# Kernel tuning notes

Hardware: AMD Instinct MI355X
Metric: run time of the kernel (lower is better)

Reference implementation:

```python
import jax, jax.numpy as jnp
import numpy as np

B, IN, H, NOPT = 16384, 4096, 128, 64
GAIN = 0.5  # default control_gains value in the module


def gru_cell(x, h, Wih, Whh, bih, bhh):
    # torch GRU single step; gate order r, z, n
    gi = x @ Wih + bih          # [B, 3H]
    gh = h @ Whh + bhh          # [B, 3H]
    ir, iz, inn = jnp.split(gi, 3, axis=-1)
    hr, hz, hn = jnp.split(gh, 3, axis=-1)
    r = jax.nn.sigmoid(ir + hr)
    z = jax.nn.sigmoid(iz + hz)
    n = jnp.tanh(inn + r * hn)
    return (1.0 - z) * n + z * h


def setup_inputs() -> dict:
    key = jax.random.key(0)
    ks = jax.random.split(key, 12)
    s = lambda k, shape: (jax.random.normal(k, shape, jnp.float32) * 0.05)
    return {
        "obs": jax.random.normal(ks[0], (B, IN), jnp.float32),
        "chosen_option": jax.random.randint(ks[1], (B,), 0, NOPT),
        "h0": jnp.zeros((B, H), jnp.float32),
        "h1": jnp.zeros((B, H), jnp.float32),
        "Wa": s(ks[2], (IN, H)), "ba": jnp.zeros((H,), jnp.float32),
        "Wih0": s(ks[3], (H, 3 * H)), "Whh0": s(ks[4], (H, 3 * H)),
        "bih0": jnp.zeros((3 * H,), jnp.float32), "bhh0": jnp.zeros((3 * H,), jnp.float32),
        "Wih1": s(ks[5], (2 * H, 3 * H)), "Whh1": s(ks[6], (H, 3 * H)),
        "bih1": jnp.zeros((3 * H,), jnp.float32), "bhh1": jnp.zeros((3 * H,), jnp.float32),
        "Wv0": s(ks[7], (H, NOPT)), "bv0": jnp.zeros((NOPT,), jnp.float32),
        "Wv1": s(ks[8], (H, NOPT)), "bv1": jnp.zeros((NOPT,), jnp.float32),
        "Wt0": s(ks[9], (H, NOPT)), "bt0": jnp.zeros((NOPT,), jnp.float32),
    }


def reference(obs, chosen_option, h0, h1, Wa, ba, Wih0, Whh0, bih0, bhh0,
              Wih1, Whh1, bih1, bhh1, Wv0, bv0, Wv1, bv1, Wt0, bt0):
    # attention: tanh(Linear(obs))
    attn = jnp.tanh(obs @ Wa + ba)                       # [B, H]
    # layer 0: GRU on attn
    h0n = gru_cell(attn, h0, Wih0, Whh0, bih0, bhh0)     # [B, H]
    hc0 = (h0n - 0.5) * GAIN + 0.5                       # gain contrast
    v0 = hc0 @ Wv0 + bv0                                 # [B, NOPT]
    term = jax.nn.sigmoid(hc0 @ Wt0 + bt0)               # [B, NOPT]
    term_p = jnp.take_along_axis(term, chosen_option[:, None], axis=1)  # [B, 1]
    # layer 1: GRU on cat(attn, own hidden)
    x1 = jnp.concatenate([attn, h1], axis=-1)            # [B, 2H]
    h1n = gru_cell(x1, h1, Wih1, Whh1, bih1, bhh1)       # [B, H]
    hc1 = (h1n - 0.5) * GAIN + 0.5
    v1 = hc1 @ Wv1 + bv1                                 # [B, NOPT]
    return v0, term_p, v1, h0n, h1n
```

## Files before the change

kernel.cpp:

```cpp
#include <hip/hip_runtime.h>
#include <stdint.h>


typedef __attribute__((ext_vector_type(8))) short bf16x8;
typedef __attribute__((ext_vector_type(4))) float f32x4;
typedef __attribute__((ext_vector_type(4))) float f4;
typedef __attribute__((ext_vector_type(4))) unsigned short u16x4;

#define INDIM 4096
#define H 128
#define NOPT 64

#define WS_WAT    0u
#define WS_WIH0T  524288u
#define WS_WHH0T  573440u
#define WS_WIH1T  622592u
#define WS_WHH1T  720896u
#define WS_WV0T   770048u
#define WS_WV1T   778240u
#define WS_WT0T   786432u
#define WS_ATTN   794624u

#define OUT_V0    0u
#define OUT_TERMP 1048576u
#define OUT_V1    1064960u
#define OUT_H0N   2113536u
#define OUT_H1N   4210688u

static __device__ __forceinline__ float bf2f(uint16_t u) {
  union { uint32_t i; float f; } x; x.i = ((uint32_t)u) << 16; return x.f;
}
static __device__ __forceinline__ uint16_t f2bf(float f) {
  union { float f; uint32_t i; } x; x.f = f;
  uint32_t r = x.i + 0x7fffu + ((x.i >> 16) & 1u);
  return (uint16_t)(r >> 16);
}
static __device__ __forceinline__ float sigm(float x) { return 1.0f / (1.0f + __expf(-x)); }
static __device__ __forceinline__ float fast_tanh(float x) {
  float e = __expf(2.0f * x);
  return 1.0f - 2.0f / (e + 1.0f);
}
static __device__ __forceinline__ f32x4 mfma16(bf16x8 a, bf16x8 b, f32x4 c) {
  return __builtin_amdgcn_mfma_f32_16x16x32_bf16(a, b, c, 0, 0, 0);
}
static __device__ __forceinline__ u16x4 pack4(f4 v) {
  u16x4 p;
  p[0] = f2bf(v[0]); p[1] = f2bf(v[1]); p[2] = f2bf(v[2]); p[3] = f2bf(v[3]);
  return p;
}

__global__ void k_transpose(const float* __restrict__ Wa,
                            const float* __restrict__ Wih0,
                            const float* __restrict__ Whh0,
                            const float* __restrict__ Wih1,
                            const float* __restrict__ Whh1,
                            const float* __restrict__ Wv0,
                            const float* __restrict__ Wv1,
                            const float* __restrict__ Wt0,
                            uint16_t* __restrict__ ws) {
  int blk = blockIdx.x;
  const float* in; uint16_t* out; int ksh; int N; int base;
  if (blk < 2048)      { in = Wa;   out = ws + WS_WAT;   ksh = 12; N = 128; base = 0; }
  else if (blk < 2240) { in = Wih0; out = ws + WS_WIH0T; ksh = 7;  N = 384; base = 2048; }
  else if (blk < 2432) { in = Whh0; out = ws + WS_WHH0T; ksh = 7;  N = 384; base = 2240; }
  else if (blk < 2816) { in = Wih1; out = ws + WS_WIH1T; ksh = 8;  N = 384; base = 2432; }
  else if (blk < 3008) { in = Whh1; out = ws + WS_WHH1T; ksh = 7;  N = 384; base = 2816; }
  else if (blk < 3040) { in = Wv0;  out = ws + WS_WV0T;  ksh = 7;  N = 64;  base = 3008; }
  else if (blk < 3072) { in = Wv1;  out = ws + WS_WV1T;  ksh = 7;  N = 64;  base = 3040; }
  else                 { in = Wt0;  out = ws + WS_WT0T;  ksh = 7;  N = 64;  base = 3072; }
  int e = (blk - base) * 256 + (int)threadIdx.x;
  int n = e >> ksh;
  int k = e & ((1 << ksh) - 1);
  out[e] = f2bf(in[(size_t)k * N + n]);
}

__launch_bounds__(128)
__global__ void k_attn(const float* __restrict__ obs,
                       uint16_t* __restrict__ ws,
                       const float* __restrict__ ba) {
  __shared__ uint16_t sA[32 * 64];
  __shared__ uint16_t sB[128 * 64];
  const uint16_t* WaT = ws + WS_WAT;
  uint16_t* attn = ws + WS_ATTN;
  const int t = threadIdx.x, w = t >> 6, lane = t & 63;
  const int l15 = lane & 15, quad = lane >> 4;
  const int row0 = blockIdx.x * 32;
  f32x4 acc[8] = {};
  const int rA = 16 * w + l15;
  for (int kt = 0; kt < 64; ++kt) {
    const int k0 = kt * 64;
    f4 va[4]; bf16x8 vb[8];
#pragma unroll
    for (int i = 0; i < 4; ++i) {
      int p = i * 128 + t, r = p >> 4, kb4 = p & 15;
      va[i] = *(const f4*)(obs + (size_t)(row0 + r) * INDIM + k0 + kb4 * 4);
    }
#pragma unroll
    for (int i = 0; i < 8; ++i) {
      int p = i * 128 + t, n = p >> 3, kb = p & 7;
      vb[i] = *(const bf16x8*)(WaT + (size_t)n * INDIM + k0 + kb * 8);
    }
    __syncthreads();
#pragma unroll
    for (int i = 0; i < 4; ++i) {
      int p = i * 128 + t, r = p >> 4, kb4 = p & 15;
      int c8 = (kb4 >> 1) ^ (r & 7);
      *(u16x4*)&sA[(r * 8 + c8) * 8 + (kb4 & 1) * 4] = pack4(va[i]);
    }
#pragma unroll
    for (int i = 0; i < 8; ++i) {
      int p = i * 128 + t, n = p >> 3, kb = p & 7;
      *(bf16x8*)&sB[(n * 8 + (kb ^ (n & 7))) * 8] = vb[i];
    }
    __syncthreads();
#pragma unroll
    for (int ks = 0; ks < 2; ++ks) {
      const int kb = ks * 4 + quad;
      bf16x8 a = *(const bf16x8*)&sA[(rA * 8 + (kb ^ (rA & 7))) * 8];
#pragma unroll
      for (int nb = 0; nb < 8; ++nb) {
        int nB = nb * 16 + l15;
        bf16x8 b = *(const bf16x8*)&sB[(nB * 8 + (kb ^ (nB & 7))) * 8];
        acc[nb] = mfma16(a, b, acc[nb]);
      }
    }
  }
#pragma unroll
  for (int nb = 0; nb < 8; ++nb) {
    int col = nb * 16 + l15;
    float bav = ba[col];
#pragma unroll
    for (int i = 0; i < 4; ++i) {
      int grow = row0 + 16 * w + quad * 4 + i;
      attn[(size_t)grow * H + col] = f2bf(fast_tanh(acc[nb][i] + bav));
    }
  }
}

__launch_bounds__(128)
__global__ void k_gru0(const uint16_t* __restrict__ ws,
                       const float* __restrict__ h0,
                       const float* __restrict__ bih0,
                       const float* __restrict__ bhh0,
                       const float* __restrict__ bv0,
                       const float* __restrict__ bt0,
                       const int* __restrict__ chosen,
                       float* __restrict__ out) {
  __shared__ uint16_t sX[32 * 128];
  __shared__ uint16_t sH[32 * 128];
  __shared__ uint16_t sC[32 * 128];
  const uint16_t* attn = ws + WS_ATTN;
  const uint16_t* WihT = ws + WS_WIH0T;
  const uint16_t* WhhT = ws + WS_WHH0T;
  const uint16_t* WvT  = ws + WS_WV0T;
  const uint16_t* WtT  = ws + WS_WT0T;
  const int t = threadIdx.x, w = t >> 6, lane = t & 63;
  const int l15 = lane & 15, quad = lane >> 4;
  const int row0 = blockIdx.x * 32;
  {
    bf16x8 vx[4]; f4 vh[8];
#pragma unroll
    for (int i = 0; i < 4; ++i) {
      int p = i * 128 + t, r = p >> 4, kb = p & 15;
      vx[i] = *(const bf16x8*)(attn + (size_t)(row0 + r) * H + kb * 8);
    }
#pragma unroll
    for (int i = 0; i < 8; ++i) {
      int p = i * 128 + t, r = p >> 5, kb4 = p & 31;
      vh[i] = *(const f4*)(h0 + (size_t)(row0 + r) * H + kb4 * 4);
    }
#pragma unroll
    for (int i = 0; i < 4; ++i) {
      int p = i * 128 + t, r = p >> 4, kb = p & 15;
      *(bf16x8*)&sX[(r * 16 + (kb ^ (r & 15))) * 8] = vx[i];
    }
#pragma unroll
    for (int i = 0; i < 8; ++i) {
      int p = i * 128 + t, r = p >> 5, kb4 = p & 31;
      int c8 = (kb4 >> 1) ^ (r & 15);
      *(u16x4*)&sH[(r * 16 + c8) * 8 + (kb4 & 1) * 4] = pack4(vh[i]);
    }
  }
  __syncthreads();
  const int rA = 16 * w + l15;
  bf16x8 ax[4], ah[4];
#pragma unroll
  for (int ks = 0; ks < 4; ++ks) {
    int kb = ks * 4 + quad;
    int sl = rA * 16 + (kb ^ (rA & 15));
    ax[ks] = *(const bf16x8*)&sX[sl * 8];
    ah[ks] = *(const bf16x8*)&sH[sl * 8];
  }
#pragma unroll
  for (int nb = 0; nb < 8; ++nb) {
    f32x4 air = {}, ahr = {}, aiz = {}, ahz = {}, ain = {}, ahn = {};
    int nrow = nb * 16 + l15;
#pragma unroll
    for (int ks = 0; ks < 4; ++ks) {
      int k = ks * 32 + quad * 8;
      bf16x8 b;
      b = *(const bf16x8*)(WihT + (size_t)(nrow      ) * H + k); air = mfma16(ax[ks], b, air);
      b = *(const bf16x8*)(WihT + (size_t)(nrow + 128) * H + k); aiz = mfma16(ax[ks], b, aiz);
      b = *(const bf16x8*)(WihT + (size_t)(nrow + 256) * H + k); ain = mfma16(ax[ks], b, ain);
      b = *(const bf16x8*)(WhhT + (size_t)(nrow      ) * H + k); ahr = mfma16(ah[ks], b, ahr);
      b = *(const bf16x8*)(WhhT + (size_t)(nrow + 128) * H + k); ahz = mfma16(ah[ks], b, ahz);
      b = *(const bf16x8*)(WhhT + (size_t)(nrow + 256) * H + k); ahn = mfma16(ah[ks], b, ahn);
    }
    int col = nb * 16 + l15;
    float b_ir = bih0[col],       b_hr = bhh0[col];
    float b_iz = bih0[col + 128], b_hz = bhh0[col + 128];
    float b_in = bih0[col + 256], b_hn = bhh0[col + 256];
    int slc = col >> 3;
#pragma unroll
    for (int i = 0; i < 4; ++i) {
      int r = 16 * w + quad * 4 + i;
      int grow = row0 + r;
      float rr = sigm(air[i] + ahr[i] + b_ir + b_hr);
      float zz = sigm(aiz[i] + ahz[i] + b_iz + b_hz);
      float nn = fast_tanh(ain[i] + b_in + rr * (ahn[i] + b_hn));
      float hv = bf2f(sH[(r * 16 + (slc ^ (r & 15))) * 8 + (col & 7)]);
      float hnew = (1.0f - zz) * nn + zz * hv;
      out[OUT_H0N + (size_t)grow * H + col] = hnew;
      sC[(r * 16 + (slc ^ (r & 15))) * 8 + (col & 7)] = f2bf(0.5f * hnew + 0.25f);
    }
  }
  __syncthreads();
  bf16x8 ac[4];
#pragma unroll
  for (int ks = 0; ks < 4; ++ks) {
    int kb = ks * 4 + quad;
    ac[ks] = *(const bf16x8*)&sC[(rA * 16 + (kb ^ (rA & 15))) * 8];
  }
#pragma unroll
  for (int vb = 0; vb < 4; ++vb) {
    f32x4 av = {}, at = {};
    int nrow = vb * 16 + l15;
#pragma unroll
    for (int ks = 0; ks < 4; ++ks) {
      int k = ks * 32 + quad * 8;
      bf16x8 b;
      b = *(const bf16x8*)(WvT + (size_t)nrow * H + k); av = mfma16(ac[ks], b, av);
      b = *(const bf16x8*)(WtT + (size_t)nrow * H + k); at = mfma16(ac[ks], b, at);
    }
    int col = vb * 16 + l15;
    float bvv = bv0[col], btv = bt0[col];
#pragma unroll
    for (int i = 0; i < 4; ++i) {
      int grow = row0 + 16 * w + quad * 4 + i;
      out[OUT_V0 + (size_t)grow * NOPT + col] = av[i] + bvv;
      if (chosen[grow] == col)
        out[OUT_TERMP + grow] = sigm(at[i] + btv);
    }
  }
}

__launch_bounds__(128)
__global__ void k_gru1(const uint16_t* __restrict__ ws,
                       const float* __restrict__ h1,
                       const float* __restrict__ bih1,
                       const float* __restrict__ bhh1,
                       const float* __restrict__ bv1,
                       float* __restrict__ out) {
  __shared__ uint16_t sX[32 * 128];
  __shared__ uint16_t sH[32 * 128];
  __shared__ uint16_t sC[32 * 128];
  const uint16_t* attn  = ws + WS_ATTN;
  const uint16_t* WihT  = ws + WS_WIH1T;
  const uint16_t* WhhT  = ws + WS_WHH1T;
  const uint16_t* WvT   = ws + WS_WV1T;
  const int t = threadIdx.x, w = t >> 6, lane = t & 63;
  const int l15 = lane & 15, quad = lane >> 4;
  const int row0 = blockIdx.x * 32;
  {
    bf16x8 vx[4]; f4 vh[8];
#pragma unroll
    for (int i = 0; i < 4; ++i) {
      int p = i * 128 + t, r = p >> 4, kb = p & 15;
      vx[i] = *(const bf16x8*)(attn + (size_t)(row0 + r) * H + kb * 8);
    }
#pragma unroll
    for (int i = 0; i < 8; ++i) {
      int p = i * 128 + t, r = p >> 5, kb4 = p & 31;
      vh[i] = *(const f4*)(h1 + (size_t)(row0 + r) * H + kb4 * 4);
    }
#pragma unroll
    for (int i = 0; i < 4; ++i) {
      int p = i * 128 + t, r = p >> 4, kb = p & 15;
      *(bf16x8*)&sX[(r * 16 + (kb ^ (r & 15))) * 8] = vx[i];
    }
#pragma unroll
    for (int i = 0; i < 8; ++i) {
      int p = i * 128 + t, r = p >> 5, kb4 = p & 31;
      int c8 = (kb4 >> 1) ^ (r & 15);
      *(u16x4*)&sH[(r * 16 + c8) * 8 + (kb4 & 1) * 4] = pack4(vh[i]);
    }
  }
  __syncthreads();
  const int rA = 16 * w + l15;
  bf16x8 ax[4], ah[4];
#pragma unroll
  for (int ks = 0; ks < 4; ++ks) {
    int kb = ks * 4 + quad;
    int sl = rA * 16 + (kb ^ (rA & 15));
    ax[ks] = *(const bf16x8*)&sX[sl * 8];
    ah[ks] = *(const bf16x8*)&sH[sl * 8];
  }
#pragma unroll
  for (int nb = 0; nb < 8; ++nb) {
    f32x4 air = {}, ahr = {}, aiz = {}, ahz = {}, ain = {}, ahn = {};
    int nrow = nb * 16 + l15;
#pragma unroll
    for (int ks = 0; ks < 8; ++ks) {
      int k = ks * 32 + quad * 8;
      bf16x8 a = (ks < 4) ? ax[ks] : ah[ks - 4];
      bf16x8 b;
      b = *(const bf16x8*)(WihT + (size_t)(nrow      ) * 256 + k); air = mfma16(a, b, air);
      b = *(const bf16x8*)(WihT + (size_t)(nrow + 128) * 256 + k); aiz = mfma16(a, b, aiz);
      b = *(const bf16x8*)(WihT + (size_t)(nrow + 256) * 256 + k); ain = mfma16(a, b, ain);
    }
#pragma unroll
    for (int ks = 0; ks < 4; ++ks) {
      int k = ks * 32 + quad * 8;
      bf16x8 b;
      b = *(const bf16x8*)(WhhT + (size_t)(nrow      ) * H + k); ahr = mfma16(ah[ks], b, ahr);
      b = *(const bf16x8*)(WhhT + (size_t)(nrow + 128) * H + k); ahz = mfma16(ah[ks], b, ahz);
      b = *(const bf16x8*)(WhhT + (size_t)(nrow + 256) * H + k); ahn = mfma16(ah[ks], b, ahn);
    }
    int col = nb * 16 + l15;
    float b_ir = bih1[col],       b_hr = bhh1[col];
    float b_iz = bih1[col + 128], b_hz = bhh1[col + 128];
    float b_in = bih1[col + 256], b_hn = bhh1[col + 256];
    int slc = col >> 3;
#pragma unroll
    for (int i = 0; i < 4; ++i) {
      int r = 16 * w + quad * 4 + i;
      int grow = row0 + r;
      float rr = sigm(air[i] + ahr[i] + b_ir + b_hr);
      float zz = sigm(aiz[i] + ahz[i] + b_iz + b_hz);
      float nn = fast_tanh(ain[i] + b_in + rr * (ahn[i] + b_hn));
      float hv = bf2f(sH[(r * 16 + (slc ^ (r & 15))) * 8 + (col & 7)]);
      float hnew = (1.0f - zz) * nn + zz * hv;
      out[OUT_H1N + (size_t)grow * H + col] = hnew;
      sC[(r * 16 + (slc ^ (r & 15))) * 8 + (col & 7)] = f2bf(0.5f * hnew + 0.25f);
    }
  }
  __syncthreads();
  bf16x8 ac[4];
#pragma unroll
  for (int ks = 0; ks < 4; ++ks) {
    int kb = ks * 4 + quad;
    ac[ks] = *(const bf16x8*)&sC[(rA * 16 + (kb ^ (rA & 15))) * 8];
  }
#pragma unroll
  for (int vb = 0; vb < 4; ++vb) {
    f32x4 av = {};
    int nrow = vb * 16 + l15;
#pragma unroll
    for (int ks = 0; ks < 4; ++ks) {
      int k = ks * 32 + quad * 8;
      bf16x8 b = *(const bf16x8*)(WvT + (size_t)nrow * H + k);
      av = mfma16(ac[ks], b, av);
    }
    int col = vb * 16 + l15;
    float bvv = bv1[col];
#pragma unroll
    for (int i = 0; i < 4; ++i) {
      int grow = row0 + 16 * w + quad * 4 + i;
      out[OUT_V1 + (size_t)grow * NOPT + col] = av[i] + bvv;
    }
  }
}

extern "C" void kernel_launch(void* const* d_in, const int* in_sizes, int n_in,
                              void* d_out, int out_size, void* d_ws, size_t ws_size,
                              hipStream_t stream) {
  (void)in_sizes; (void)n_in; (void)out_size; (void)ws_size;
  const float* obs    = (const float*)d_in[0];
  const int*   chosen = (const int*)d_in[1];
  const float* h0     = (const float*)d_in[2];
  const float* h1     = (const float*)d_in[3];
  const float* Wa     = (const float*)d_in[4];
  const float* ba     = (const float*)d_in[5];
  const float* Wih0   = (const float*)d_in[6];
  const float* Whh0   = (const float*)d_in[7];
  const float* bih0   = (const float*)d_in[8];
  const float* bhh0   = (const float*)d_in[9];
  const float* Wih1   = (const float*)d_in[10];
  const float* Whh1   = (const float*)d_in[11];
  const float* bih1   = (const float*)d_in[12];
  const float* bhh1   = (const float*)d_in[13];
  const float* Wv0    = (const float*)d_in[14];
  const float* bv0    = (const float*)d_in[15];
  const float* Wv1    = (const float*)d_in[16];
  const float* bv1    = (const float*)d_in[17];
  const float* Wt0    = (const float*)d_in[18];
  const float* bt0    = (const float*)d_in[19];
  uint16_t* ws  = (uint16_t*)d_ws;
  float*    out = (float*)d_out;

  hipLaunchKernelGGL(k_transpose, dim3(3104), dim3(256), 0, stream,
                     Wa, Wih0, Whh0, Wih1, Whh1, Wv0, Wv1, Wt0, ws);
  hipLaunchKernelGGL(k_attn, dim3(512), dim3(128), 0, stream, obs, ws, ba);
  hipLaunchKernelGGL(k_gru0, dim3(512), dim3(128), 0, stream,
                     ws, h0, bih0, bhh0, bv0, bt0, chosen, out);
  hipLaunchKernelGGL(k_gru1, dim3(512), dim3(128), 0, stream,
                     ws, h1, bih1, bhh1, bv1, out);
}
```

Baseline: 544.2 us.

## Fuse attention and both GRU layers into one per-wave kernel

Merges the attention GEMM, GRU layer 0 with its value/termination heads, and GRU layer 1 with its value head into one kernel. Each wave owns 16 rows and keeps attention activations in per-wave shared memory, so the bf16 attention buffer no longer makes a round trip through global memory and two launches go away. The attention GEMM now loads obs and WaT straight from global memory into registers, with no shared-memory staging and no block barriers. The cost is that B fragments are re-read from global/L2 by every wave instead of being shared across the block, and register pressure is higher.

```diff
diff --git a/kernel.cpp b/kernel.cpp
--- a/kernel.cpp
+++ b/kernel.cpp
@@ -4,8 +4,7 @@
 
 typedef __attribute__((ext_vector_type(8))) short bf16x8;
 typedef __attribute__((ext_vector_type(4))) float f32x4;
-typedef __attribute__((ext_vector_type(4))) float f4;
-typedef __attribute__((ext_vector_type(4))) unsigned short u16x4;
+typedef __attribute__((ext_vector_type(8))) float f32x8;
 
 #define INDIM 4096
 #define H 128
@@ -19,7 +18,6 @@
 #define WS_WV0T   770048u
 #define WS_WV1T   778240u
 #define WS_WT0T   786432u
-#define WS_ATTN   794624u
 
 #define OUT_V0    0u
 #define OUT_TERMP 1048576u
@@ -27,9 +25,6 @@
 #define OUT_H0N   2113536u
 #define OUT_H1N   4210688u
 
-static __device__ __forceinline__ float bf2f(uint16_t u) {
-  union { uint32_t i; float f; } x; x.i = ((uint32_t)u) << 16; return x.f;
-}
 static __device__ __forceinline__ uint16_t f2bf(float f) {
   union { float f; uint32_t i; } x; x.f = f;
   uint32_t r = x.i + 0x7fffu + ((x.i >> 16) & 1u);
@@ -43,10 +38,11 @@
 static __device__ __forceinline__ f32x4 mfma16(bf16x8 a, bf16x8 b, f32x4 c) {
   return __builtin_amdgcn_mfma_f32_16x16x32_bf16(a, b, c, 0, 0, 0);
 }
-static __device__ __forceinline__ u16x4 pack4(f4 v) {
-  u16x4 p;
-  p[0] = f2bf(v[0]); p[1] = f2bf(v[1]); p[2] = f2bf(v[2]); p[3] = f2bf(v[3]);
-  return p;
+static __device__ __forceinline__ bf16x8 cvt8(f32x8 v) {
+  bf16x8 r;
+#pragma unroll
+  for (int j = 0; j < 8; ++j) r[j] = (short)f2bf(v[j]);
+  return r;
 }
 
 __global__ void k_transpose(const float* __restrict__ Wa,
@@ -75,298 +71,215 @@
 }
 
 __launch_bounds__(128)
-__global__ void k_attn(const float* __restrict__ obs,
-                       uint16_t* __restrict__ ws,
-                       const float* __restrict__ ba) {
-  __shared__ uint16_t sA[32 * 64];
-  __shared__ uint16_t sB[128 * 64];
-  const uint16_t* WaT = ws + WS_WAT;
-  uint16_t* attn = ws + WS_ATTN;
+__global__ void k_fused(const float* __restrict__ obs,
+                        const uint16_t* __restrict__ ws,
+                        const float* __restrict__ ba,
+                        const float* __restrict__ h0,
+                        const float* __restrict__ bih0,
+                        const float* __restrict__ bhh0,
+                        const float* __restrict__ bv0,
+                        const float* __restrict__ bt0,
+                        const int* __restrict__ chosen,
+                        const float* __restrict__ h1,
+                        const float* __restrict__ bih1,
+                        const float* __restrict__ bhh1,
+                        const float* __restrict__ bv1,
+                        float* __restrict__ out) {
+  __shared__ uint16_t sAttn[2][16 * 16 * 8];
+  __shared__ uint16_t sHC[2][16 * 16 * 8];
+  const uint16_t* WaT   = ws + WS_WAT;
+  const uint16_t* Wih0T = ws + WS_WIH0T;
+  const uint16_t* Whh0T = ws + WS_WHH0T;
+  const uint16_t* Wih1T = ws + WS_WIH1T;
+  const uint16_t* Whh1T = ws + WS_WHH1T;
+  const uint16_t* Wv0T  = ws + WS_WV0T;
+  const uint16_t* Wv1T  = ws + WS_WV1T;
+  const uint16_t* Wt0T  = ws + WS_WT0T;
   const int t = threadIdx.x, w = t >> 6, lane = t & 63;
   const int l15 = lane & 15, quad = lane >> 4;
-  const int row0 = blockIdx.x * 32;
+  const int row0 = blockIdx.x * 32 + w * 16;
+  uint16_t* sX = sAttn[w];
+  uint16_t* sC = sHC[w];
+
   f32x4 acc[8] = {};
-  const int rA = 16 * w + l15;
-  for (int kt = 0; kt < 64; ++kt) {
-    const int k0 = kt * 64;
-    f4 va[4]; bf16x8 vb[8];
+  {
+    const float* arow = obs + (size_t)(row0 + l15) * INDIM + quad * 8;
+    const uint16_t* brow = WaT + (size_t)l15 * INDIM + quad * 8;
+#pragma unroll 2
+    for (int kt = 0; kt < 64; ++kt) {
+      const int k0 = kt * 64;
+      f32x8 av0 = *(const f32x8*)(arow + k0);
+      f32x8 av1 = *(const f32x8*)(arow + k0 + 32);
+      bf16x8 a0 = cvt8(av0);
+      bf16x8 a1 = cvt8(av1);
+#pragma unroll
+      for (int nb = 0; nb < 8; ++nb) {
+        const uint16_t* bp = brow + (size_t)(nb * 16) * INDIM + k0;
+        bf16x8 b0 = *(const bf16x8*)(bp);
+        bf16x8 b1 = *(const bf16x8*)(bp + 32);
+        acc[nb] = mfma16(a0, b0, acc[nb]);
+        acc[nb] = mfma16(a1, b1, acc[nb]);
+      }
+    }
+  }
+#pragma unroll
+  for (int nb = 0; nb < 8; ++nb) {
+    const int col = nb * 16 + l15;
+    const float bav = ba[col];
+    const int kb = col >> 3;
 #pragma unroll
     for (int i = 0; i < 4; ++i) {
-      int p = i * 128 + t, r = p >> 4, kb4 = p & 15;
-      va[i] = *(const f4*)(obs + (size_t)(row0 + r) * INDIM + k0 + kb4 * 4);
-    }
-#pragma unroll
-    for (int i = 0; i < 8; ++i) {
-      int p = i * 128 + t, n = p >> 3, kb = p & 7;
-      vb[i] = *(const bf16x8*)(WaT + (size_t)n * INDIM + k0 + kb * 8);
-    }
-    __syncthreads();
-#pragma unroll
-    for (int i = 0; i < 4; ++i) {
-      int p = i * 128 + t, r = p >> 4, kb4 = p & 15;
-      int c8 = (kb4 >> 1) ^ (r & 7);
-      *(u16x4*)&sA[(r * 8 + c8) * 8 + (kb4 & 1) * 4] = pack4(va[i]);
-    }
-#pragma unroll
-    for (int i = 0; i < 8; ++i) {
-      int p = i * 128 + t, n = p >> 3, kb = p & 7;
-      *(bf16x8*)&sB[(n * 8 + (kb ^ (n & 7))) * 8] = vb[i];
-    }
-    __syncthreads();
-#pragma unroll
-    for (int ks = 0; ks < 2; ++ks) {
+      const int r = quad * 4 + i;
+      sX[(r * 16 + (kb ^ r)) * 8 + (col & 7)] = f2bf(fast_tanh(acc[nb][i] + bav));
+    }
+  }
+
+  bf16x8 ax[4], ah[4];
+  {
+    const float* hrow = h0 + (size_t)(row0 + l15) * H + quad * 8;
+#pragma unroll
+    for (int ks = 0; ks < 4; ++ks) {
       const int kb = ks * 4 + quad;
-      bf16x8 a = *(const bf16x8*)&sA[(rA * 8 + (kb ^ (rA & 7))) * 8];
-#pragma unroll
-      for (int nb = 0; nb < 8; ++nb) {
-        int nB = nb * 16 + l15;
-        bf16x8 b = *(const bf16x8*)&sB[(nB * 8 + (kb ^ (nB & 7))) * 8];
-        acc[nb] = mfma16(a, b, acc[nb]);
-      }
-    }
-  }
-#pragma unroll
-  for (int nb = 0; nb < 8; ++nb) {
-    int col = nb * 16 + l15;
-    float bav = ba[col];
-#pragma unroll
-    for (int i = 0; i < 4; ++i) {
-      int grow = row0 + 16 * w + quad * 4 + i;
-      attn[(size_t)grow * H + col] = f2bf(fast_tanh(acc[nb][i] + bav));
-    }
-  }
-}
-
-__launch_bounds__(128)
-__global__ void k_gru0(const uint16_t* __restrict__ ws,
-                       const float* __restrict__ h0,
-                       const float* __restrict__ bih0,
-                       const float* __restrict__ bhh0,
-                       const float* __restrict__ bv0,
-                       const float* __restrict__ bt0,
-                       const int* __restrict__ chosen,
-                       float* __restrict__ out) {
-  __shared__ uint16_t sX[32 * 128];
-  __shared__ uint16_t sH[32 * 128];
-  __shared__ uint16_t sC[32 * 128];
-  const uint16_t* attn = ws + WS_ATTN;
-  const uint16_t* WihT = ws + WS_WIH0T;
-  const uint16_t* WhhT = ws + WS_WHH0T;
-  const uint16_t* WvT  = ws + WS_WV0T;
-  const uint16_t* WtT  = ws + WS_WT0T;
-  const int t = threadIdx.x, w = t >> 6, lane = t & 63;
-  const int l15 = lane & 15, quad = lane >> 4;
-  const int row0 = blockIdx.x * 32;
-  {
-    bf16x8 vx[4]; f4 vh[8];
-#pragma unroll
-    for (int i = 0; i < 4; ++i) {
-      int p = i * 128 + t, r = p >> 4, kb = p & 15;
-      vx[i] = *(const bf16x8*)(attn + (size_t)(row0 + r) * H + kb * 8);
-    }
-#pragma unroll
-    for (int i = 0; i < 8; ++i) {
-      int p = i * 128 + t, r = p >> 5, kb4 = p & 31;
-      vh[i] = *(const f4*)(h0 + (size_t)(row0 + r) * H + kb4 * 4);
-    }
-#pragma unroll
-    for (int i = 0; i < 4; ++i) {
-      int p = i * 128 + t, r = p >> 4, kb = p & 15;
-      *(bf16x8*)&sX[(r * 16 + (kb ^ (r & 15))) * 8] = vx[i];
-    }
-#pragma unroll
-    for (int i = 0; i < 8; ++i) {
-      int p = i * 128 + t, r = p >> 5, kb4 = p & 31;
-      int c8 = (kb4 >> 1) ^ (r & 15);
-      *(u16x4*)&sH[(r * 16 + c8) * 8 + (kb4 & 1) * 4] = pack4(vh[i]);
-    }
-  }
-  __syncthreads();
-  const int rA = 16 * w + l15;
-  bf16x8 ax[4], ah[4];
-#pragma unroll
-  for (int ks = 0; ks < 4; ++ks) {
-    int kb = ks * 4 + quad;
-    int sl = rA * 16 + (kb ^ (rA & 15));
-    ax[ks] = *(const bf16x8*)&sX[sl * 8];
-    ah[ks] = *(const bf16x8*)&sH[sl * 8];
+      ax[ks] = *(const bf16x8*)&sX[(l15 * 16 + (kb ^ l15)) * 8];
+      ah[ks] = cvt8(*(const f32x8*)(hrow + ks * 32));
+    }
   }
 #pragma unroll
   for (int nb = 0; nb < 8; ++nb) {
     f32x4 air = {}, ahr = {}, aiz = {}, ahz = {}, ain = {}, ahn = {};
-    int nrow = nb * 16 + l15;
-#pragma unroll
-    for (int ks = 0; ks < 4; ++ks) {
-      int k = ks * 32 + quad * 8;
+    const int nrow = nb * 16 + l15;
+#pragma unroll
+    for (int ks = 0; ks < 4; ++ks) {
+      const int k = ks * 32 + quad * 8;
       bf16x8 b;
-      b = *(const bf16x8*)(WihT + (size_t)(nrow      ) * H + k); air = mfma16(ax[ks], b, air);
-      b = *(const bf16x8*)(WihT + (size_t)(nrow + 128) * H + k); aiz = mfma16(ax[ks], b, aiz);
-      b = *(const bf16x8*)(WihT + (size_t)(nrow + 256) * H + k); ain = mfma16(ax[ks], b, ain);
-      b = *(const bf16x8*)(WhhT + (size_t)(nrow      ) * H + k); ahr = mfma16(ah[ks], b, ahr);
-      b = *(const bf16x8*)(WhhT + (size_t)(nrow + 128) * H + k); ahz = mfma16(ah[ks], b, ahz);
-      b = *(const bf16x8*)(WhhT + (size_t)(nrow + 256) * H + k); ahn = mfma16(ah[ks], b, ahn);
-    }
-    int col = nb * 16 + l15;
-    float b_ir = bih0[col],       b_hr = bhh0[col];
-    float b_iz = bih0[col + 128], b_hz = bhh0[col + 128];
-    float b_in = bih0[col + 256], b_hn = bhh0[col + 256];
-    int slc = col >> 3;
+      b = *(const bf16x8*)(Wih0T + (size_t)(nrow      ) * H + k); air = mfma16(ax[ks], b, air);
+      b = *(const bf16x8*)(Wih0T + (size_t)(nrow + 128) * H + k); aiz = mfma16(ax[ks], b, aiz);
+      b = *(const bf16x8*)(Wih0T + (size_t)(nrow + 256) * H + k); ain = mfma16(ax[ks], b, ain);
+      b = *(const bf16x8*)(Whh0T + (size_t)(nrow      ) * H + k); ahr = mfma16(ah[ks], b, ahr);
+      b = *(const bf16x8*)(Whh0T + (size_t)(nrow + 128) * H + k); ahz = mfma16(ah[ks], b, ahz);
+      b = *(const bf16x8*)(Whh0T + (size_t)(nrow + 256) * H + k); ahn = mfma16(ah[ks], b, ahn);
+    }
+    const int col = nrow;
+    const float b_ir = bih0[col],       b_hr = bhh0[col];
+    const float b_iz = bih0[col + 128], b_hz = bhh0[col + 128];
+    const float b_in = bih0[col + 256], b_hn = bhh0[col + 256];
+    const int kb = col >> 3;
 #pragma unroll
     for (int i = 0; i < 4; ++i) {
-      int r = 16 * w + quad * 4 + i;
-      int grow = row0 + r;
-      float rr = sigm(air[i] + ahr[i] + b_ir + b_hr);
-      float zz = sigm(aiz[i] + ahz[i] + b_iz + b_hz);
-      float nn = fast_tanh(ain[i] + b_in + rr * (ahn[i] + b_hn));
-      float hv = bf2f(sH[(r * 16 + (slc ^ (r & 15))) * 8 + (col & 7)]);
-      float hnew = (1.0f - zz) * nn + zz * hv;
+      const int r = quad * 4 + i;
+      const int grow = row0 + r;
+      const float rr = sigm(air[i] + ahr[i] + b_ir + b_hr);
+      const float zz = sigm(aiz[i] + ahz[i] + b_iz + b_hz);
+      const float nn = fast_tanh(ain[i] + b_in + rr * (ahn[i] + b_hn));
+      const float hv = h0[(size_t)grow * H + col];
+      const float hnew = (1.0f - zz) * nn + zz * hv;
       out[OUT_H0N + (size_t)grow * H + col] = hnew;
-      sC[(r * 16 + (slc ^ (r & 15))) * 8 + (col & 7)] = f2bf(0.5f * hnew + 0.25f);
-    }
-  }
-  __syncthreads();
-  bf16x8 ac[4];
-#pragma unroll
-  for (int ks = 0; ks < 4; ++ks) {
-    int kb = ks * 4 + quad;
-    ac[ks] = *(const bf16x8*)&sC[(rA * 16 + (kb ^ (rA & 15))) * 8];
-  }
-#pragma unroll
-  for (int vb = 0; vb < 4; ++vb) {
-    f32x4 av = {}, at = {};
-    int nrow = vb * 16 + l15;
-#pragma unroll
-    for (int ks = 0; ks < 4; ++ks) {
-      int k = ks * 32 + quad * 8;
-      bf16x8 b;
-      b = *(const bf16x8*)(WvT + (size_t)nrow * H + k); av = mfma16(ac[ks], b, av);
-      b = *(const bf16x8*)(WtT + (size_t)nrow * H + k); at = mfma16(ac[ks], b, at);
-    }
-    int col = vb * 16 + l15;
-    float bvv = bv0[col], btv = bt0[col];
-#pragma unroll
-    for (int i = 0; i < 4; ++i) {
-      int grow = row0 + 16 * w + quad * 4 + i;
-      out[OUT_V0 + (size_t)grow * NOPT + col] = av[i] + bvv;
-      if (chosen[grow] == col)
-        out[OUT_TERMP + grow] = sigm(at[i] + btv);
-    }
-  }
-}
-
-__launch_bounds__(128)
-__global__ void k_gru1(const uint16_t* __restrict__ ws,
-                       const float* __restrict__ h1,
-                       const float* __restrict__ bih1,
-                       const float* __restrict__ bhh1,
-                       const float* __restrict__ bv1,
-                       float* __restrict__ out) {
-  __shared__ uint16_t sX[32 * 128];
-  __shared__ uint16_t sH[32 * 128];
-  __shared__ uint16_t sC[32 * 128];
-  const uint16_t* attn  = ws + WS_ATTN;
-  const uint16_t* WihT  = ws + WS_WIH1T;
-  const uint16_t* WhhT  = ws + WS_WHH1T;
-  const uint16_t* WvT   = ws + WS_WV1T;
-  const int t = threadIdx.x, w = t >> 6, lane = t & 63;
-  const int l15 = lane & 15, quad = lane >> 4;
-  const int row0 = blockIdx.x * 32;
-  {
-    bf16x8 vx[4]; f4 vh[8];
-#pragma unroll
-    for (int i = 0; i < 4; ++i) {
-      int p = i * 128 + t, r = p >> 4, kb = p & 15;
-      vx[i] = *(const bf16x8*)(attn + (size_t)(row0 + r) * H + kb * 8);
-    }
-#pragma unroll
-    for (int i = 0; i < 8; ++i) {
-      int p = i * 128 + t, r = p >> 5, kb4 = p & 31;
-      vh[i] = *(const f4*)(h1 + (size_t)(row0 + r) * H + kb4 * 4);
-    }
-#pragma unroll
-    for (int i = 0; i < 4; ++i) {
-      int p = i * 128 + t, r = p >> 4, kb = p & 15;
-      *(bf16x8*)&sX[(r * 16 + (kb ^ (r & 15))) * 8] = vx[i];
-    }
-#pragma unroll
-    for (int i = 0; i < 8; ++i) {
-      int p = i * 128 + t, r = p >> 5, kb4 = p & 31;
-      int c8 = (kb4 >> 1) ^ (r & 15);
-      *(u16x4*)&sH[(r * 16 + c8) * 8 + (kb4 & 1) * 4] = pack4(vh[i]);
-    }
-  }
-  __syncthreads();
-  const int rA = 16 * w + l15;
-  bf16x8 ax[4], ah[4];
-#pragma unroll
-  for (int ks = 0; ks < 4; ++ks) {
-    int kb = ks * 4 + quad;
-    int sl = rA * 16 + (kb ^ (rA & 15));
-    ax[ks] = *(const bf16x8*)&sX[sl * 8];
-    ah[ks] = *(const bf16x8*)&sH[sl * 8];
+      sC[(r * 16 + (kb ^ r)) * 8 + (col & 7)] = f2bf(0.5f * hnew + 0.25f);
+    }
+  }
+  {
+    int ch[4];
+#pragma unroll
+    for (int i = 0; i < 4; ++i) ch[i] = chosen[row0 + quad * 4 + i];
+    bf16x8 ac[4];
+#pragma unroll
+    for (int ks = 0; ks < 4; ++ks) {
+      const int kb = ks * 4 + quad;
+      ac[ks] = *(const bf16x8*)&sC[(l15 * 16 + (kb ^ l15)) * 8];
+    }
+#pragma unroll
+    for (int vb = 0; vb < 4; ++vb) {
+      f32x4 av = {}, at = {};
+      const int nrow = vb * 16 + l15;
+#pragma unroll
+      for (int ks = 0; ks < 4; ++ks) {
+        const int k = ks * 32 + quad * 8;
+        bf16x8 b;
+        b = *(const bf16x8*)(Wv0T + (size_t)nrow * H + k); av = mfma16(ac[ks], b, av);
+        b = *(const bf16x8*)(Wt0T + (size_t)nrow * H + k); at = mfma16(ac[ks], b, at);
+      }
+      const int col = vb * 16 + l15;
+      const float bvv = bv0[col], btv = bt0[col];
+#pragma unroll
+      for (int i = 0; i < 4; ++i) {
+        const int grow = row0 + quad * 4 + i;
+        out[OUT_V0 + (size_t)grow * NOPT + col] = av[i] + bvv;
+        if (ch[i] == col)
+          out[OUT_TERMP + grow] = sigm(at[i] + btv);
+      }
+    }
+  }
+
+  bf16x8 ah1[4];
+  {
+    const float* hrow = h1 + (size_t)(row0 + l15) * H + quad * 8;
+#pragma unroll
+    for (int ks = 0; ks < 4; ++ks)
+      ah1[ks] = cvt8(*(const f32x8*)(hrow + ks * 32));
   }
 #pragma unroll
   for (int nb = 0; nb < 8; ++nb) {
     f32x4 air = {}, ahr = {}, aiz = {}, ahz = {}, ain = {}, ahn = {};
-    int nrow = nb * 16 + l15;
+    const int nrow = nb * 16 + l15;
 #pragma unroll
     for (int ks = 0; ks < 8; ++ks) {
-      int k = ks * 32 + quad * 8;
-      bf16x8 a = (ks < 4) ? ax[ks] : ah[ks - 4];
+      const int k = ks * 32 + quad * 8;
+      const bf16x8 a = (ks < 4) ? ax[ks] : ah1[ks - 4];
       bf16x8 b;
-      b = *(const bf16x8*)(WihT + (size_t)(nrow      ) * 256 + k); air = mfma16(a, b, air);
-      b = *(const bf16x8*)(WihT + (size_t)(nrow + 128) * 256 + k); aiz = mfma16(a, b, aiz);
-      b = *(const bf16x8*)(WihT + (size_t)(nrow + 256) * 256 + k); ain = mfma16(a, b, ain);
-    }
-#pragma unroll
-    for (int ks = 0; ks < 4; ++ks) {
-      int k = ks * 32 + quad * 8;
+      b = *(const bf16x8*)(Wih1T + (size_t)(nrow      ) * 256 + k); air = mfma16(a, b, air);
+      b = *(const bf16x8*)(Wih1T + (size_t)(nrow + 128) * 256 + k); aiz = mfma16(a, b, aiz);
+      b = *(const bf16x8*)(Wih1T + (size_t)(nrow + 256) * 256 + k); ain = mfma16(a, b, ain);
+    }
+#pragma unroll
+    for (int ks = 0; ks < 4; ++ks) {
+      const int k = ks * 32 + quad * 8;
       bf16x8 b;
-      b = *(const bf16x8*)(WhhT + (size_t)(nrow      ) * H + k); ahr = mfma16(ah[ks], b, ahr);
-      b = *(const bf16x8*)(WhhT + (size_t)(nrow + 128) * H + k); ahz = mfma16(ah[ks], b, ahz);
-      b = *(const bf16x8*)(WhhT + (size_t)(nrow + 256) * H + k); ahn = mfma16(ah[ks], b, ahn);
-    }
-    int col = nb * 16 + l15;
-    float b_ir = bih1[col],       b_hr = bhh1[col];
-    float b_iz = bih1[col + 128], b_hz = bhh1[col + 128];
-    float b_in = bih1[col + 256], b_hn = bhh1[col + 256];
-    int slc = col >> 3;
+      b = *(const bf16x8*)(Whh1T + (size_t)(nrow      ) * H + k); ahr = mfma16(ah1[ks], b, ahr);
+      b = *(const bf16x8*)(Whh1T + (size_t)(nrow + 128) * H + k); ahz = mfma16(ah1[ks], b, ahz);
+      b = *(const bf16x8*)(Whh1T + (size_t)(nrow + 256) * H + k); ahn = mfma16(ah1[ks], b, ahn);
+    }
+    const int col = nrow;
+    const float b_ir = bih1[col],       b_hr = bhh1[col];
+    const float b_iz = bih1[col + 128], b_hz = bhh1[col + 128];
+    const float b_in = bih1[col + 256], b_hn = bhh1[col + 256];
+    const int kb = col >> 3;
 #pragma unroll
     for (int i = 0; i < 4; ++i) {
-      int r = 16 * w + quad * 4 + i;
-      int grow = row0 + r;
-      float rr = sigm(air[i] + ahr[i] + b_ir + b_hr);
-      float zz = sigm(aiz[i] + ahz[i] + b_iz + b_hz);
-      float nn = fast_tanh(ain[i] + b_in + rr * (ahn[i] + b_hn));
-      float hv = bf2f(sH[(r * 16 + (slc ^ (r & 15))) * 8 + (col & 7)]);
-      float hnew = (1.0f - zz) * nn + zz * hv;
+      const int r = quad * 4 + i;
+      const int grow = row0 + r;
+      const float rr = sigm(air[i] + ahr[i] + b_ir + b_hr);
+      const float zz = sigm(aiz[i] + ahz[i] + b_iz + b_hz);
+      const float nn = fast_tanh(ain[i] + b_in + rr * (ahn[i] + b_hn));
+      const float hv = h1[(size_t)grow * H + col];
+      const float hnew = (1.0f - zz) * nn + zz * hv;
       out[OUT_H1N + (size_t)grow * H + col] = hnew;
-      sC[(r * 16 + (slc ^ (r & 15))) * 8 + (col & 7)] = f2bf(0.5f * hnew + 0.25f);
-    }
-  }
-  __syncthreads();
-  bf16x8 ac[4];
-#pragma unroll
-  for (int ks = 0; ks < 4; ++ks) {
-    int kb = ks * 4 + quad;
-    ac[ks] = *(const bf16x8*)&sC[(rA * 16 + (kb ^ (rA & 15))) * 8];
-  }
-#pragma unroll
-  for (int vb = 0; vb < 4; ++vb) {
-    f32x4 av = {};
-    int nrow = vb * 16 + l15;
-#pragma unroll
-    for (int ks = 0; ks < 4; ++ks) {
-      int k = ks * 32 + quad * 8;
-      bf16x8 b = *(const bf16x8*)(WvT + (size_t)nrow * H + k);
-      av = mfma16(ac[ks], b, av);
-    }
-    int col = vb * 16 + l15;
-    float bvv = bv1[col];
-#pragma unroll
-    for (int i = 0; i < 4; ++i) {
-      int grow = row0 + 16 * w + quad * 4 + i;
-      out[OUT_V1 + (size_t)grow * NOPT + col] = av[i] + bvv;
+      sC[(r * 16 + (kb ^ r)) * 8 + (col & 7)] = f2bf(0.5f * hnew + 0.25f);
+    }
+  }
+  {
+    bf16x8 ac[4];
+#pragma unroll
+    for (int ks = 0; ks < 4; ++ks) {
+      const int kb = ks * 4 + quad;
+      ac[ks] = *(const bf16x8*)&sC[(l15 * 16 + (kb ^ l15)) * 8];
+    }
+#pragma unroll
+    for (int vb = 0; vb < 4; ++vb) {
+      f32x4 av = {};
+      const int nrow = vb * 16 + l15;
+#pragma unroll
+      for (int ks = 0; ks < 4; ++ks) {
+        const int k = ks * 32 + quad * 8;
+        bf16x8 b = *(const bf16x8*)(Wv1T + (size_t)nrow * H + k);
+        av = mfma16(ac[ks], b, av);
+      }
+      const int col = vb * 16 + l15;
+      const float bvv = bv1[col];
+#pragma unroll
+      for (int i = 0; i < 4; ++i) {
+        const int grow = row0 + quad * 4 + i;
+        out[OUT_V1 + (size_t)grow * NOPT + col] = av[i] + bvv;
+      }
     }
   }
 }
@@ -400,9 +313,7 @@
 
   hipLaunchKernelGGL(k_transpose, dim3(3104), dim3(256), 0, stream,
                      Wa, Wih0, Whh0, Wih1, Whh1, Wv0, Wv1, Wt0, ws);
-  hipLaunchKernelGGL(k_attn, dim3(512), dim3(128), 0, stream, obs, ws, ba);
-  hipLaunchKernelGGL(k_gru0, dim3(512), dim3(128), 0, stream,
-                     ws, h0, bih0, bhh0, bv0, bt0, chosen, out);
-  hipLaunchKernelGGL(k_gru1, dim3(512), dim3(128), 0, stream,
-                     ws, h1, bih1, bhh1, bv1, out);
-}
+  hipLaunchKernelGGL(k_fused, dim3(512), dim3(128), 0, stream,
+                     obs, ws, ba, h0, bih0, bhh0, bv0, bt0, chosen,
+                     h1, bih1, bhh1, bv1, out);
+}
```

Result: no change. 539.3 us (-0.9%).
